# Kernel optimization log

Hardware: AMD Instinct MI355X
Metric: run time of the kernel (lower is better)

## Reference

```python
import jax, jax.numpy as jnp
import numpy as np

B, C, H, W = 8, 256, 64, 64
NUM_LABELS = 16  # labels in {-1, 0..15}; -1 means 'no group'


def setup_inputs() -> dict:
    key = jax.random.key(0)
    kx, kl, kw, kb = jax.random.split(key, 4)
    x = jax.random.normal(kx, (B, C, H, W), dtype=jnp.float32)
    # labels in [-1, NUM_LABELS)
    labels = jax.random.randint(kl, (B * C,), 0, NUM_LABELS + 1) - 1
    # groups=C, kernel 1x1: conv weight is (3C,1,1,1) -> per-output-channel scale; bias (3C,)
    w = jax.random.normal(kw, (3 * C,), dtype=jnp.float32) * 0.5
    b = jax.random.normal(kb, (3 * C,), dtype=jnp.float32) * 0.02
    return {"x": x, "labels": labels, "w": w, "b": b}


def reference(x, labels, w, b):
    # x: (B,C,h,w); labels: (B*C,); w,b: (3C,)
    Bv, Cv, hv, wv = x.shape
    hw = hv * wv
    xf = x.reshape(Bv, Cv, hw)
    # grouped 1x1 conv: out channel o (of 3C) reads input channel o//3
    x_rep = jnp.repeat(xf, 3, axis=1)                      # (B,3C,hw)
    qkv = x_rep * w[None, :, None] + b[None, :, None]      # (B,3C,hw)
    flat = qkv.reshape(Bv * 3 * Cv, hw)                    # matches torch reshape(1,3BC,hw)
    BC = Bv * Cv
    q, k, v = flat[:BC], flat[BC:2 * BC], flat[2 * BC:]    # each (BC, hw)
    valid = labels != -1                                   # (BC,)
    same = (labels[:, None] == labels[None, :]) & valid[:, None] & valid[None, :]
    # per-label-group attention == masked dense attention (softmax over same-label cols only)
    scores = q @ k.T                                       # (BC, BC), no sqrt(d) scaling (as in source)
    neg = jnp.finfo(scores.dtype).min
    scores = jnp.where(same, scores, neg)
    weights = jax.nn.softmax(scores, axis=-1)
    out = weights @ v                                      # (BC, hw)
    out = jnp.where(valid[:, None], out, jnp.zeros((), out.dtype))  # -1 rows stay zero
    return out[None]                                       # (1, BC, hw)
```

## Files before the change

### kernel.cpp

```cpp
#include <hip/hip_runtime.h>
#include <cfloat>

#define B_   8
#define C_   256
#define HW_  4096
#define BC_  2048
#define TC_  768
#define NG_  16
#define MAXG 320
#define UK0  682
#define NUQ  683
#define NUK  684
#define NXU  1366

#define SPLITK 8
#define NT     11
#define NTILES (NT * NT)
#define KSL    (HW_ / SPLITK)
#define WKC    (KSL / 4)
#define NP1    (NUQ * NUK)

#define MCAP  192
#define CST   192
#define BKP   216

typedef __attribute__((ext_vector_type(8))) short short8;
typedef __attribute__((ext_vector_type(4))) float floatx4;

__global__ __launch_bounds__(256) void group_build_kernel(
    const int* __restrict__ labels, int* __restrict__ grp_n,
    int* __restrict__ members, int* __restrict__ posArr)
{
  __shared__ int lab[BC_];
  __shared__ int cnts[256];
  const int g = blockIdx.x;
  const int t = threadIdx.x;
  for (int idx = t; idx < BC_; idx += 256) lab[idx] = labels[idx];
  __syncthreads();

  const int base = t * 8;
  int cnt = 0;
#pragma unroll
  for (int k = 0; k < 8; k++) cnt += (lab[base + k] == g) ? 1 : 0;
  cnts[t] = cnt;
  for (int off = 1; off < 256; off <<= 1) {
    __syncthreads();
    const int v = (t >= off) ? cnts[t - off] : 0;
    __syncthreads();
    cnts[t] += v;
  }
  __syncthreads();
  int pos = cnts[t] - cnt;
  if (t == 255) grp_n[g] = cnts[255] < MAXG ? cnts[255] : MAXG;
#pragma unroll
  for (int k = 0; k < 8; k++) {
    const int i = base + k;
    if (lab[i] == g) {
      if (pos < MAXG) { members[g * MAXG + pos] = i; posArr[i] = pos; }
      pos++;
    }
  }
}

__device__ __forceinline__ unsigned short f32_to_bf16_rne(float f) {
  unsigned u = __float_as_uint(f);
  unsigned r = (u + 0x7FFFu + ((u >> 16) & 1u)) >> 16;
  return (unsigned short)r;
}

__global__ __launch_bounds__(256) void conv_kernel(
    const float* __restrict__ x, unsigned short* __restrict__ xhi,
    unsigned short* __restrict__ xlo, float* __restrict__ sums)
{
  const int u = blockIdx.x;
  const int t = threadIdx.x;
  unsigned short* hrow = xhi + (size_t)u * HW_;
  unsigned short* lrow = xlo + (size_t)u * HW_;
  const float* row = x + (size_t)u * HW_;
  float s = 0.f;
#pragma unroll
  for (int i = 0; i < 4; i++) {
    const int col = i * 1024 + t * 4;
    const float4 v = *(const float4*)(row + col);
    s += v.x + v.y + v.z + v.w;
    ushort4 h, l;
    h.x = f32_to_bf16_rne(v.x);
    h.y = f32_to_bf16_rne(v.y);
    h.z = f32_to_bf16_rne(v.z);
    h.w = f32_to_bf16_rne(v.w);
    l.x = f32_to_bf16_rne(v.x - __uint_as_float((unsigned)h.x << 16));
    l.y = f32_to_bf16_rne(v.y - __uint_as_float((unsigned)h.y << 16));
    l.z = f32_to_bf16_rne(v.z - __uint_as_float((unsigned)h.z << 16));
    l.w = f32_to_bf16_rne(v.w - __uint_as_float((unsigned)h.w << 16));
    *(ushort4*)(hrow + col) = h;
    *(ushort4*)(lrow + col) = l;
  }
#pragma unroll
  for (int o = 32; o > 0; o >>= 1) s += __shfl_down(s, o);
  __shared__ float red[4];
  if ((t & 63) == 0) red[t >> 6] = s;
  __syncthreads();
  if (t == 0) sums[u] = red[0] + red[1] + red[2] + red[3];
}

__global__ __launch_bounds__(256) void gram_mfma_kernel(
    const unsigned short* __restrict__ xhi, const unsigned short* __restrict__ xlo,
    float* __restrict__ P)
{
  const int bid  = blockIdx.x;
  const int z    = bid & 7;
  const int tile = bid >> 3;
  const int m0 = (tile % NT) * 64;
  const int n0 = (tile / NT) * 64;

  const int t = threadIdx.x;
  const int wave = t >> 6;
  const int lane = t & 63;
  const int fr = lane & 15;
  const int fq = lane >> 4;

  const int kbase = z * KSL + wave * WKC + fq * 8;
  const unsigned short *pah[4], *pal[4], *pbh[4], *pbl[4];
#pragma unroll
  for (int i = 0; i < 4; i++) {
    const int ar = min(m0 + fr + i * 16, NUQ - 1);
    const int br = min(UK0 + n0 + fr + i * 16, NXU - 1);
    pah[i] = xhi + (size_t)ar * HW_ + kbase;
    pal[i] = xlo + (size_t)ar * HW_ + kbase;
    pbh[i] = xhi + (size_t)br * HW_ + kbase;
    pbl[i] = xlo + (size_t)br * HW_ + kbase;
  }

  floatx4 acc[4][4];
#pragma unroll
  for (int i = 0; i < 4; i++)
#pragma unroll
    for (int j = 0; j < 4; j++) acc[i][j] = (floatx4)(0.f);

  for (int kk = 0; kk < WKC; kk += 32) {
    short8 ah[4], al[4], bh[4], bl[4];
#pragma unroll
    for (int i = 0; i < 4; i++) {
      ah[i] = *(const short8*)(pah[i] + kk);
      al[i] = *(const short8*)(pal[i] + kk);
      bh[i] = *(const short8*)(pbh[i] + kk);
      bl[i] = *(const short8*)(pbl[i] + kk);
    }
#pragma unroll
    for (int mt = 0; mt < 4; mt++)
#pragma unroll
      for (int nt = 0; nt < 4; nt++) {
        acc[mt][nt] = __builtin_amdgcn_mfma_f32_16x16x32_bf16(ah[mt], bh[nt], acc[mt][nt], 0, 0, 0);
        acc[mt][nt] = __builtin_amdgcn_mfma_f32_16x16x32_bf16(al[mt], bh[nt], acc[mt][nt], 0, 0, 0);
        acc[mt][nt] = __builtin_amdgcn_mfma_f32_16x16x32_bf16(ah[mt], bl[nt], acc[mt][nt], 0, 0, 0);
      }
  }

  __shared__ float R[2][64][68];
  float* R0 = &R[0][0][0];
  float* R1 = &R[1][0][0];
  if (wave == 0 || wave == 2) {
    float* Rw = (wave == 0) ? R0 : R1;
#pragma unroll
    for (int mt = 0; mt < 4; mt++)
#pragma unroll
      for (int nt = 0; nt < 4; nt++)
#pragma unroll
        for (int r = 0; r < 4; r++)
          Rw[(mt * 16 + fq * 4 + r) * 68 + nt * 16 + fr] = acc[mt][nt][r];
  }
  __syncthreads();
  if (wave == 1 || wave == 3) {
    float* Rw = (wave == 1) ? R0 : R1;
#pragma unroll
    for (int mt = 0; mt < 4; mt++)
#pragma unroll
      for (int nt = 0; nt < 4; nt++)
#pragma unroll
        for (int r = 0; r < 4; r++)
          Rw[(mt * 16 + fq * 4 + r) * 68 + nt * 16 + fr] += acc[mt][nt][r];
  }
  __syncthreads();
  const int em = t >> 2;
  const int en = (t & 3) * 16;
  const int gm = m0 + em;
  if (gm < NUQ) {
    float* dst = P + (size_t)z * NP1 + (size_t)gm * NUK + n0;
#pragma unroll
    for (int i4 = 0; i4 < 4; i4++) {
      const int n = en + i4 * 4;
      if (n0 + n < NUK) {
        float4 v;
        v.x = R0[em * 68 + n + 0] + R1[em * 68 + n + 0];
        v.y = R0[em * 68 + n + 1] + R1[em * 68 + n + 1];
        v.z = R0[em * 68 + n + 2] + R1[em * 68 + n + 2];
        v.w = R0[em * 68 + n + 3] + R1[em * 68 + n + 3];
        *(float4*)(dst + n) = v;
      }
    }
  }
}

__global__ __launch_bounds__(256) void gram_reduce_kernel(
    const float* __restrict__ P, float* __restrict__ S)
{
  const int idx = (blockIdx.x * 256 + threadIdx.x) * 4;
  if (idx < NP1) {
    float4 s = *(const float4*)(P + idx);
#pragma unroll
    for (int sl = 1; sl < SPLITK; sl++) {
      const float4 a = *(const float4*)(P + (size_t)sl * NP1 + idx);
      s.x += a.x; s.y += a.y; s.z += a.z; s.w += a.w;
    }
    *(float4*)(S + idx) = s;
  }
}

__device__ __forceinline__ float blockReduceMax(float v, float* red) {
#pragma unroll
  for (int o = 32; o > 0; o >>= 1) v = fmaxf(v, __shfl_down(v, o));
  if ((threadIdx.x & 63) == 0) red[threadIdx.x >> 6] = v;
  __syncthreads();
  v = fmaxf(fmaxf(red[0], red[1]), fmaxf(red[2], red[3]));
  __syncthreads();
  return v;
}
__device__ __forceinline__ float blockReduceSum(float v, float* red) {
#pragma unroll
  for (int o = 32; o > 0; o >>= 1) v += __shfl_down(v, o);
  if ((threadIdx.x & 63) == 0) red[threadIdx.x >> 6] = v;
  __syncthreads();
  v = red[0] + red[1] + red[2] + red[3];
  __syncthreads();
  return v;
}

__global__ __launch_bounds__(256) void softmax_kernel(
    const int* __restrict__ labels, const float* __restrict__ w,
    const float* __restrict__ bbias, const float* __restrict__ sums,
    const float* __restrict__ S, const int* __restrict__ grp_n,
    const int* __restrict__ members, const int* __restrict__ posArr,
    unsigned short* __restrict__ coefh, float* __restrict__ cb,
    float* __restrict__ out)
{
  const int i = blockIdx.x;
  const int t = threadIdx.x;
  const int g = labels[i];
  if (g < 0) {
    const float4 z = make_float4(0.f, 0.f, 0.f, 0.f);
    float4* orow = (float4*)(out + (size_t)i * HW_);
    for (int cidx = t; cidx < HW_ / 4; cidx += 256) orow[cidx] = z;
    return;
  }
  __shared__ float red[4];
  const int n   = grp_n[g];
  const int jq  = i % TC_;
  const int uqi = (i / TC_) * C_ + jq / 3;
  const float wq = w[jq], bq = bbias[jq];
  const float sq = sums[uqi];
  const float* Srow = S + (size_t)uqi * NUK;

  const int jj0 = t, jj1 = t + 256;
  float s0 = -FLT_MAX, s1 = -FLT_MAX;
  if (jj0 < n) {
    const int j = members[g * MAXG + jj0];
    const int rk = j + BC_;
    const int jk = rk % TC_;
    const int uk = (rk / TC_) * C_ + jk / 3;
    s0 = wq * w[jk] * Srow[uk - UK0] + (wq * bbias[jk]) * sq +
         (bq * w[jk]) * sums[uk] + (bq * bbias[jk]) * 4096.f;
  }
  if (jj1 < n) {
    const int j = members[g * MAXG + jj1];
    const int rk = j + BC_;
    const int jk = rk % TC_;
    const int uk = (rk / TC_) * C_ + jk / 3;
    s1 = wq * w[jk] * Srow[uk - UK0] + (wq * bbias[jk]) * sq +
         (bq * w[jk]) * sums[uk] + (bq * bbias[jk]) * 4096.f;
  }
  const float mx = blockReduceMax(fmaxf(s0, s1), red);
  const float e0 = (jj0 < n) ? expf(s0 - mx) : 0.f;
  const float e1 = (jj1 < n) ? expf(s1 - mx) : 0.f;
  const float tot = blockReduceSum(e0 + e1, red);
  const float inv = 1.f / tot;

  const int pos = posArr[i];
  unsigned short* crow = coefh + ((size_t)g * MCAP + pos) * CST;
  float lcb = 0.f;
  if (jj0 < n) {
    const int j = members[g * MAXG + jj0];
    const int jv = (j + 2 * BC_) % TC_;
    const float wgt = e0 * inv;
    if (pos < MCAP && jj0 < CST) crow[jj0] = f32_to_bf16_rne(wgt * w[jv]);
    lcb += wgt * bbias[jv];
  } else if (pos < MCAP && jj0 < CST) {
    crow[jj0] = 0;
  }
  if (jj1 < n) {
    const int j = members[g * MAXG + jj1];
    const int jv = (j + 2 * BC_) % TC_;
    const float wgt = e1 * inv;
    lcb += wgt * bbias[jv];
  }
  const float cbi = blockReduceSum(lcb, red);
  if (t == 0) cb[i] = cbi;
}

__global__ __launch_bounds__(256) void out_mfma_kernel(
    const float* __restrict__ x, const unsigned short* __restrict__ coefh,
    const float* __restrict__ cb, const int* __restrict__ grp_n,
    const int* __restrict__ members, float* __restrict__ out)
{
  const int g  = blockIdx.x;
  const int c0 = blockIdx.y * 64;
  const int n  = min(grp_n[g], MCAP);
  if (n == 0) return;
  const int Kceil = (n + 31) & ~31;
  const int nk8 = Kceil >> 3;
  const int t = threadIdx.x;
  const int wave = t >> 6;
  const int lane = t & 63;
  const int fr = lane & 15;
  const int fq = lane >> 4;

  __shared__ unsigned short Bt[64][BKP];
  __shared__ int   mem[MCAP];
  __shared__ float cbs[MCAP];

  if (t < n) {
    const int j = members[g * MAXG + t];
    mem[t] = j;
    cbs[t] = cb[j];
  }
  __syncthreads();

  {
    const int colq = t & 15;
    const int kcb  = t >> 4;
    for (int kc = kcb; kc < nk8; kc += 16) {
      float4 vals[8];
#pragma unroll
      for (int j = 0; j < 8; j++) {
        const int k = kc * 8 + j;
        if (k < n) {
          const int jm = mem[k];
          const int rv = jm + 2 * BC_;
          const int uv = (rv / TC_) * C_ + (rv % TC_) / 3;
          vals[j] = *(const float4*)(x + (size_t)uv * HW_ + c0 + colq * 4);
        } else {
          vals[j] = make_float4(0.f, 0.f, 0.f, 0.f);
        }
      }
#pragma unroll
      for (int c = 0; c < 4; c++) {
        short8 pk;
        pk[0] = (short)f32_to_bf16_rne(c == 0 ? vals[0].x : c == 1 ? vals[0].y : c == 2 ? vals[0].z : vals[0].w);
        pk[1] = (short)f32_to_bf16_rne(c == 0 ? vals[1].x : c == 1 ? vals[1].y : c == 2 ? vals[1].z : vals[1].w);
        pk[2] = (short)f32_to_bf16_rne(c == 0 ? vals[2].x : c == 1 ? vals[2].y : c == 2 ? vals[2].z : vals[2].w);
        pk[3] = (short)f32_to_bf16_rne(c == 0 ? vals[3].x : c == 1 ? vals[3].y : c == 2 ? vals[3].z : vals[3].w);
        pk[4] = (short)f32_to_bf16_rne(c == 0 ? vals[4].x : c == 1 ? vals[4].y : c == 2 ? vals[4].z : vals[4].w);
        pk[5] = (short)f32_to_bf16_rne(c == 0 ? vals[5].x : c == 1 ? vals[5].y : c == 2 ? vals[5].z : vals[5].w);
        pk[6] = (short)f32_to_bf16_rne(c == 0 ? vals[6].x : c == 1 ? vals[6].y : c == 2 ? vals[6].z : vals[6].w);
        pk[7] = (short)f32_to_bf16_rne(c == 0 ? vals[7].x : c == 1 ? vals[7].y : c == 2 ? vals[7].z : vals[7].w);
        *(short8*)&Bt[colq * 4 + c][kc * 8] = pk;
      }
    }
  }
  __syncthreads();

  const int colw = wave * 16 + fr;

  for (int m0 = 0; m0 < n; m0 += 32) {
    floatx4 acc0 = (floatx4)(0.f), acc1 = (floatx4)(0.f);
    const unsigned short* pa0 = coefh + ((size_t)g * MCAP + m0 + fr) * CST + fq * 8;
    const unsigned short* pa1 = pa0 + 16 * CST;
    for (int k = 0; k < Kceil; k += 32) {
      const short8 a0 = *(const short8*)(pa0 + k);
      const short8 a1 = *(const short8*)(pa1 + k);
      const short8 b  = *(const short8*)&Bt[colw][fq * 8 + k];
      acc0 = __builtin_amdgcn_mfma_f32_16x16x32_bf16(a0, b, acc0, 0, 0, 0);
      acc1 = __builtin_amdgcn_mfma_f32_16x16x32_bf16(a1, b, acc1, 0, 0, 0);
    }
#pragma unroll
    for (int r = 0; r < 4; r++) {
      int m = m0 + fq * 4 + r;
      if (m < n) out[(size_t)mem[m] * HW_ + c0 + colw] = acc0[r] + cbs[m];
      m += 16;
      if (m < n) out[(size_t)mem[m] * HW_ + c0 + colw] = acc1[r] + cbs[m];
    }
  }
}

extern "C" void kernel_launch(void* const* d_in, const int* in_sizes, int n_in,
                              void* d_out, int out_size, void* d_ws, size_t ws_size,
                              hipStream_t stream)
{
  const float* x      = (const float*)d_in[0];
  const int*   labels = (const int*)d_in[1];
  const float* w      = (const float*)d_in[2];
  const float* bb     = (const float*)d_in[3];
  float* out = (float*)d_out;

  char* wsb = (char*)d_ws;
  size_t off = 0;
  auto carve = [&](size_t bytes) -> void* {
    off = (off + 255) & ~(size_t)255;
    void* p = wsb + off;
    off += bytes;
    return p;
  };
  float* sums    = (float*)carve(NXU * sizeof(float));
  float* S       = (float*)carve((size_t)NP1 * sizeof(float));
  float* P       = (float*)carve((size_t)SPLITK * NP1 * sizeof(float));
  int*   grp_n   = (int*)carve(NG_ * sizeof(int));
  int*   members = (int*)carve((size_t)NG_ * MAXG * sizeof(int));
  int*   posArr  = (int*)carve(BC_ * sizeof(int));
  unsigned short* coefh = (unsigned short*)carve((size_t)NG_ * MCAP * CST * sizeof(unsigned short));
  float* cb      = (float*)carve(BC_ * sizeof(float));
  unsigned short* xhi = (unsigned short*)carve((size_t)NXU * HW_ * sizeof(unsigned short));
  unsigned short* xlo = (unsigned short*)carve((size_t)NXU * HW_ * sizeof(unsigned short));

  conv_kernel<<<NXU, 256, 0, stream>>>(x, xhi, xlo, sums);
  group_build_kernel<<<NG_, 256, 0, stream>>>(labels, grp_n, members, posArr);
  gram_mfma_kernel<<<NTILES * SPLITK, 256, 0, stream>>>(xhi, xlo, P);
  gram_reduce_kernel<<<(NP1 / 4 + 255) / 256, 256, 0, stream>>>(P, S);
  softmax_kernel<<<BC_, 256, 0, stream>>>(labels, w, bb, sums, S, grp_n,
                                          members, posArr, coefh, cb, out);
  out_mfma_kernel<<<dim3(NG_, HW_ / 64), 256, 0, stream>>>(
      x, coefh, cb, grp_n, members, out);
}
```

Measured before the change: 163.9 us.

## Merge prep kernels, precompute per-group key tables, reuse bf16 x in output GEMM

Result: no change. 162.1 us (-1.1%).

```diff
diff --git a/kernel.cpp b/kernel.cpp
--- a/kernel.cpp
+++ b/kernel.cpp
@@ -12,6 +12,7 @@
 #define NUQ  683
 #define NUK  684
 #define NXU  1366
+#define NXALL 2048
 
 #define SPLITK 8
 #define NT     11
@@ -19,6 +20,7 @@
 #define KSL    (HW_ / SPLITK)
 #define WKC    (KSL / 4)
 #define NP1    (NUQ * NUK)
+#define REDBLK ((NP1 / 4 + 255) / 256)
 
 #define MCAP  192
 #define CST   192
@@ -26,41 +28,6 @@
 
 typedef __attribute__((ext_vector_type(8))) short short8;
 typedef __attribute__((ext_vector_type(4))) float floatx4;
-
-__global__ __launch_bounds__(256) void group_build_kernel(
-    const int* __restrict__ labels, int* __restrict__ grp_n,
-    int* __restrict__ members, int* __restrict__ posArr)
-{
-  __shared__ int lab[BC_];
-  __shared__ int cnts[256];
-  const int g = blockIdx.x;
-  const int t = threadIdx.x;
-  for (int idx = t; idx < BC_; idx += 256) lab[idx] = labels[idx];
-  __syncthreads();
-
-  const int base = t * 8;
-  int cnt = 0;
-#pragma unroll
-  for (int k = 0; k < 8; k++) cnt += (lab[base + k] == g) ? 1 : 0;
-  cnts[t] = cnt;
-  for (int off = 1; off < 256; off <<= 1) {
-    __syncthreads();
-    const int v = (t >= off) ? cnts[t - off] : 0;
-    __syncthreads();
-    cnts[t] += v;
-  }
-  __syncthreads();
-  int pos = cnts[t] - cnt;
-  if (t == 255) grp_n[g] = cnts[255] < MAXG ? cnts[255] : MAXG;
-#pragma unroll
-  for (int k = 0; k < 8; k++) {
-    const int i = base + k;
-    if (lab[i] == g) {
-      if (pos < MAXG) { members[g * MAXG + pos] = i; posArr[i] = pos; }
-      pos++;
-    }
-  }
-}
 
 __device__ __forceinline__ unsigned short f32_to_bf16_rne(float f) {
   unsigned u = __float_as_uint(f);
@@ -68,39 +35,86 @@
   return (unsigned short)r;
 }
 
-__global__ __launch_bounds__(256) void conv_kernel(
-    const float* __restrict__ x, unsigned short* __restrict__ xhi,
-    unsigned short* __restrict__ xlo, float* __restrict__ sums)
-{
-  const int u = blockIdx.x;
+__global__ __launch_bounds__(256) void prep_kernel(
+    const float* __restrict__ x, const int* __restrict__ labels,
+    unsigned short* __restrict__ xhi, unsigned short* __restrict__ xlo,
+    float* __restrict__ sums, int* __restrict__ grp_n,
+    int* __restrict__ members, int* __restrict__ posArr, int nhi)
+{
   const int t = threadIdx.x;
+  if (blockIdx.x < NG_) {
+    __shared__ int lab[BC_];
+    __shared__ int cnts[256];
+    const int g = blockIdx.x;
+    for (int idx = t; idx < BC_; idx += 256) lab[idx] = labels[idx];
+    __syncthreads();
+    const int base = t * 8;
+    int cnt = 0;
+#pragma unroll
+    for (int k = 0; k < 8; k++) cnt += (lab[base + k] == g) ? 1 : 0;
+    cnts[t] = cnt;
+    for (int off = 1; off < 256; off <<= 1) {
+      __syncthreads();
+      const int v = (t >= off) ? cnts[t - off] : 0;
+      __syncthreads();
+      cnts[t] += v;
+    }
+    __syncthreads();
+    int pos = cnts[t] - cnt;
+    if (t == 255) grp_n[g] = cnts[255] < MAXG ? cnts[255] : MAXG;
+#pragma unroll
+    for (int k = 0; k < 8; k++) {
+      const int i = base + k;
+      if (lab[i] == g) {
+        if (pos < MAXG) { members[g * MAXG + pos] = i; posArr[i] = pos; }
+        pos++;
+      }
+    }
+    return;
+  }
+
+  const int u = blockIdx.x - NG_;
+  const float* row = x + (size_t)u * HW_;
   unsigned short* hrow = xhi + (size_t)u * HW_;
-  unsigned short* lrow = xlo + (size_t)u * HW_;
-  const float* row = x + (size_t)u * HW_;
-  float s = 0.f;
-#pragma unroll
-  for (int i = 0; i < 4; i++) {
-    const int col = i * 1024 + t * 4;
-    const float4 v = *(const float4*)(row + col);
-    s += v.x + v.y + v.z + v.w;
-    ushort4 h, l;
-    h.x = f32_to_bf16_rne(v.x);
-    h.y = f32_to_bf16_rne(v.y);
-    h.z = f32_to_bf16_rne(v.z);
-    h.w = f32_to_bf16_rne(v.w);
-    l.x = f32_to_bf16_rne(v.x - __uint_as_float((unsigned)h.x << 16));
-    l.y = f32_to_bf16_rne(v.y - __uint_as_float((unsigned)h.y << 16));
-    l.z = f32_to_bf16_rne(v.z - __uint_as_float((unsigned)h.z << 16));
-    l.w = f32_to_bf16_rne(v.w - __uint_as_float((unsigned)h.w << 16));
-    *(ushort4*)(hrow + col) = h;
-    *(ushort4*)(lrow + col) = l;
-  }
-#pragma unroll
-  for (int o = 32; o > 0; o >>= 1) s += __shfl_down(s, o);
-  __shared__ float red[4];
-  if ((t & 63) == 0) red[t >> 6] = s;
-  __syncthreads();
-  if (t == 0) sums[u] = red[0] + red[1] + red[2] + red[3];
+  if (u < NXU) {
+    unsigned short* lrow = xlo + (size_t)u * HW_;
+    float s = 0.f;
+#pragma unroll
+    for (int i = 0; i < 4; i++) {
+      const int col = i * 1024 + t * 4;
+      const float4 v = *(const float4*)(row + col);
+      s += v.x + v.y + v.z + v.w;
+      ushort4 h, l;
+      h.x = f32_to_bf16_rne(v.x);
+      h.y = f32_to_bf16_rne(v.y);
+      h.z = f32_to_bf16_rne(v.z);
+      h.w = f32_to_bf16_rne(v.w);
+      l.x = f32_to_bf16_rne(v.x - __uint_as_float((unsigned)h.x << 16));
+      l.y = f32_to_bf16_rne(v.y - __uint_as_float((unsigned)h.y << 16));
+      l.z = f32_to_bf16_rne(v.z - __uint_as_float((unsigned)h.z << 16));
+      l.w = f32_to_bf16_rne(v.w - __uint_as_float((unsigned)h.w << 16));
+      *(ushort4*)(hrow + col) = h;
+      *(ushort4*)(lrow + col) = l;
+    }
+#pragma unroll
+    for (int o = 32; o > 0; o >>= 1) s += __shfl_down(s, o);
+    __shared__ float red[4];
+    if ((t & 63) == 0) red[t >> 6] = s;
+    __syncthreads();
+    if (t == 0) sums[u] = red[0] + red[1] + red[2] + red[3];
+  } else {
+#pragma unroll
+    for (int i = 0; i < 4; i++) {
+      const int col = i * 1024 + t * 4;
+      const float4 v = *(const float4*)(row + col);
+      ushort4 h;
+      h.x = f32_to_bf16_rne(v.x);
+      h.y = f32_to_bf16_rne(v.y);
+      h.z = f32_to_bf16_rne(v.z);
+      h.w = f32_to_bf16_rne(v.w);
+      *(ushort4*)(hrow + col) = h;
+    }
+  }
 }
 
 __global__ __launch_bounds__(256) void gram_mfma_kernel(
@@ -201,18 +215,38 @@
   }
 }
 
-__global__ __launch_bounds__(256) void gram_reduce_kernel(
-    const float* __restrict__ P, float* __restrict__ S)
-{
-  const int idx = (blockIdx.x * 256 + threadIdx.x) * 4;
-  if (idx < NP1) {
-    float4 s = *(const float4*)(P + idx);
-#pragma unroll
-    for (int sl = 1; sl < SPLITK; sl++) {
-      const float4 a = *(const float4*)(P + (size_t)sl * NP1 + idx);
-      s.x += a.x; s.y += a.y; s.z += a.z; s.w += a.w;
-    }
-    *(float4*)(S + idx) = s;
+__global__ __launch_bounds__(256) void reduce_tab_kernel(
+    const float* __restrict__ P, float* __restrict__ S,
+    const float* __restrict__ w, const float* __restrict__ bbias,
+    const float* __restrict__ sums, const int* __restrict__ grp_n,
+    const int* __restrict__ members, float4* __restrict__ gtA,
+    float2* __restrict__ gtB)
+{
+  const int bid = blockIdx.x;
+  const int t = threadIdx.x;
+  if (bid < REDBLK) {
+    const int idx = (bid * 256 + t) * 4;
+    if (idx < NP1) {
+      float4 s = *(const float4*)(P + idx);
+#pragma unroll
+      for (int sl = 1; sl < SPLITK; sl++) {
+        const float4 a = *(const float4*)(P + (size_t)sl * NP1 + idx);
+        s.x += a.x; s.y += a.y; s.z += a.z; s.w += a.w;
+      }
+      *(float4*)(S + idx) = s;
+    }
+    return;
+  }
+  const int g = bid - REDBLK;
+  const int n = grp_n[g];
+  for (int p = t; p < n; p += 256) {
+    const int j = members[g * MAXG + p];
+    const int rk = j + BC_;
+    const int jk = rk % TC_;
+    const int uk = (rk / TC_) * C_ + jk / 3;
+    const int jv = (j + 2 * BC_) % TC_;
+    gtA[g * MAXG + p] = make_float4(w[jk], bbias[jk], sums[uk], w[jv]);
+    gtB[g * MAXG + p] = make_float2(bbias[jv], __int_as_float(uk - UK0));
   }
 }
 
@@ -239,9 +273,9 @@
     const int* __restrict__ labels, const float* __restrict__ w,
     const float* __restrict__ bbias, const float* __restrict__ sums,
     const float* __restrict__ S, const int* __restrict__ grp_n,
-    const int* __restrict__ members, const int* __restrict__ posArr,
-    unsigned short* __restrict__ coefh, float* __restrict__ cb,
-    float* __restrict__ out)
+    const int* __restrict__ posArr, const float4* __restrict__ gtA,
+    const float2* __restrict__ gtB, unsigned short* __restrict__ coefh,
+    float* __restrict__ cb, float* __restrict__ out)
 {
   const int i = blockIdx.x;
   const int t = threadIdx.x;
@@ -261,22 +295,19 @@
   const float* Srow = S + (size_t)uqi * NUK;
 
   const int jj0 = t, jj1 = t + 256;
+  float4 A0, A1; float2 B0, B1;
   float s0 = -FLT_MAX, s1 = -FLT_MAX;
   if (jj0 < n) {
-    const int j = members[g * MAXG + jj0];
-    const int rk = j + BC_;
-    const int jk = rk % TC_;
-    const int uk = (rk / TC_) * C_ + jk / 3;
-    s0 = wq * w[jk] * Srow[uk - UK0] + (wq * bbias[jk]) * sq +
-         (bq * w[jk]) * sums[uk] + (bq * bbias[jk]) * 4096.f;
+    A0 = gtA[g * MAXG + jj0];
+    B0 = gtB[g * MAXG + jj0];
+    s0 = wq * A0.x * Srow[__float_as_int(B0.y)] + (wq * A0.y) * sq +
+         (bq * A0.x) * A0.z + (bq * A0.y) * 4096.f;
   }
   if (jj1 < n) {
-    const int j = members[g * MAXG + jj1];
-    const int rk = j + BC_;
-    const int jk = rk % TC_;
-    const int uk = (rk / TC_) * C_ + jk / 3;
-    s1 = wq * w[jk] * Srow[uk - UK0] + (wq * bbias[jk]) * sq +
-         (bq * w[jk]) * sums[uk] + (bq * bbias[jk]) * 4096.f;
+    A1 = gtA[g * MAXG + jj1];
+    B1 = gtB[g * MAXG + jj1];
+    s1 = wq * A1.x * Srow[__float_as_int(B1.y)] + (wq * A1.y) * sq +
+         (bq * A1.x) * A1.z + (bq * A1.y) * 4096.f;
   }
   const float mx = blockReduceMax(fmaxf(s0, s1), red);
   const float e0 = (jj0 < n) ? expf(s0 - mx) : 0.f;
@@ -288,26 +319,23 @@
   unsigned short* crow = coefh + ((size_t)g * MCAP + pos) * CST;
   float lcb = 0.f;
   if (jj0 < n) {
-    const int j = members[g * MAXG + jj0];
-    const int jv = (j + 2 * BC_) % TC_;
     const float wgt = e0 * inv;
-    if (pos < MCAP && jj0 < CST) crow[jj0] = f32_to_bf16_rne(wgt * w[jv]);
-    lcb += wgt * bbias[jv];
+    if (pos < MCAP && jj0 < CST) crow[jj0] = f32_to_bf16_rne(wgt * A0.w);
+    lcb += wgt * B0.x;
   } else if (pos < MCAP && jj0 < CST) {
     crow[jj0] = 0;
   }
   if (jj1 < n) {
-    const int j = members[g * MAXG + jj1];
-    const int jv = (j + 2 * BC_) % TC_;
     const float wgt = e1 * inv;
-    lcb += wgt * bbias[jv];
+    lcb += wgt * B1.x;
   }
   const float cbi = blockReduceSum(lcb, red);
   if (t == 0) cb[i] = cbi;
 }
 
 __global__ __launch_bounds__(256) void out_mfma_kernel(
-    const float* __restrict__ x, const unsigned short* __restrict__ coefh,
+    const float* __restrict__ x, const unsigned short* __restrict__ xh,
+    const unsigned short* __restrict__ coefh,
     const float* __restrict__ cb, const int* __restrict__ grp_n,
     const int* __restrict__ members, float* __restrict__ out)
 {
@@ -338,31 +366,60 @@
     const int colq = t & 15;
     const int kcb  = t >> 4;
     for (int kc = kcb; kc < nk8; kc += 16) {
-      float4 vals[8];
-#pragma unroll
-      for (int j = 0; j < 8; j++) {
-        const int k = kc * 8 + j;
-        if (k < n) {
-          const int jm = mem[k];
-          const int rv = jm + 2 * BC_;
-          const int uv = (rv / TC_) * C_ + (rv % TC_) / 3;
-          vals[j] = *(const float4*)(x + (size_t)uv * HW_ + c0 + colq * 4);
-        } else {
-          vals[j] = make_float4(0.f, 0.f, 0.f, 0.f);
+      if (xh) {
+        ushort4 hv[8];
+#pragma unroll
+        for (int j = 0; j < 8; j++) {
+          const int k = kc * 8 + j;
+          if (k < n) {
+            const int jm = mem[k];
+            const int rv = jm + 2 * BC_;
+            const int uv = (rv / TC_) * C_ + (rv % TC_) / 3;
+            hv[j] = *(const ushort4*)(xh + (size_t)uv * HW_ + c0 + colq * 4);
+          } else {
+            hv[j] = make_ushort4(0, 0, 0, 0);
+          }
         }
-      }
-#pragma unroll
-      for (int c = 0; c < 4; c++) {
-        short8 pk;
-        pk[0] = (short)f32_to_bf16_rne(c == 0 ? vals[0].x : c == 1 ? vals[0].y : c == 2 ? vals[0].z : vals[0].w);
-        pk[1] = (short)f32_to_bf16_rne(c == 0 ? vals[1].x : c == 1 ? vals[1].y : c == 2 ? vals[1].z : vals[1].w);
-        pk[2] = (short)f32_to_bf16_rne(c == 0 ? vals[2].x : c == 1 ? vals[2].y : c == 2 ? vals[2].z : vals[2].w);
-        pk[3] = (short)f32_to_bf16_rne(c == 0 ? vals[3].x : c == 1 ? vals[3].y : c == 2 ? vals[3].z : vals[3].w);
-        pk[4] = (short)f32_to_bf16_rne(c == 0 ? vals[4].x : c == 1 ? vals[4].y : c == 2 ? vals[4].z : vals[4].w);
-        pk[5] = (short)f32_to_bf16_rne(c == 0 ? vals[5].x : c == 1 ? vals[5].y : c == 2 ? vals[5].z : vals[5].w);
-        pk[6] = (short)f32_to_bf16_rne(c == 0 ? vals[6].x : c == 1 ? vals[6].y : c == 2 ? vals[6].z : vals[6].w);
-        pk[7] = (short)f32_to_bf16_rne(c == 0 ? vals[7].x : c == 1 ? vals[7].y : c == 2 ? vals[7].z : vals[7].w);
-        *(short8*)&Bt[colq * 4 + c][kc * 8] = pk;
+#pragma unroll
+        for (int c = 0; c < 4; c++) {
+          short8 pk;
+          pk[0] = (short)(c == 0 ? hv[0].x : c == 1 ? hv[0].y : c == 2 ? hv[0].z : hv[0].w);
+          pk[1] = (short)(c == 0 ? hv[1].x : c == 1 ? hv[1].y : c == 2 ? hv[1].z : hv[1].w);
+          pk[2] = (short)(c == 0 ? hv[2].x : c == 1 ? hv[2].y : c == 2 ? hv[2].z : hv[2].w);
+          pk[3] = (short)(c == 0 ? hv[3].x : c == 1 ? hv[3].y : c == 2 ? hv[3].z : hv[3].w);
+          pk[4] = (short)(c == 0 ? hv[4].x : c == 1 ? hv[4].y : c == 2 ? hv[4].z : hv[4].w);
+          pk[5] = (short)(c == 0 ? hv[5].x : c == 1 ? hv[5].y : c == 2 ? hv[5].z : hv[5].w);
+          pk[6] = (short)(c == 0 ? hv[6].x : c == 1 ? hv[6].y : c == 2 ? hv[6].z : hv[6].w);
+          pk[7] = (short)(c == 0 ? hv[7].x : c == 1 ? hv[7].y : c == 2 ? hv[7].z : hv[7].w);
+          *(short8*)&Bt[colq * 4 + c][kc * 8] = pk;
+        }
+      } else {
+        float4 vals[8];
+#pragma unroll
+        for (int j = 0; j < 8; j++) {
+          const int k = kc * 8 + j;
+          if (k < n) {
+            const int jm = mem[k];
+            const int rv = jm + 2 * BC_;
+            const int uv = (rv / TC_) * C_ + (rv % TC_) / 3;
+            vals[j] = *(const float4*)(x + (size_t)uv * HW_ + c0 + colq * 4);
+          } else {
+            vals[j] = make_float4(0.f, 0.f, 0.f, 0.f);
+          }
+        }
+#pragma unroll
+        for (int c = 0; c < 4; c++) {
+          short8 pk;
+          pk[0] = (short)f32_to_bf16_rne(c == 0 ? vals[0].x : c == 1 ? vals[0].y : c == 2 ? vals[0].z : vals[0].w);
+          pk[1] = (short)f32_to_bf16_rne(c == 0 ? vals[1].x : c == 1 ? vals[1].y : c == 2 ? vals[1].z : vals[1].w);
+          pk[2] = (short)f32_to_bf16_rne(c == 0 ? vals[2].x : c == 1 ? vals[2].y : c == 2 ? vals[2].z : vals[2].w);
+          pk[3] = (short)f32_to_bf16_rne(c == 0 ? vals[3].x : c == 1 ? vals[3].y : c == 2 ? vals[3].z : vals[3].w);
+          pk[4] = (short)f32_to_bf16_rne(c == 0 ? vals[4].x : c == 1 ? vals[4].y : c == 2 ? vals[4].z : vals[4].w);
+          pk[5] = (short)f32_to_bf16_rne(c == 0 ? vals[5].x : c == 1 ? vals[5].y : c == 2 ? vals[5].z : vals[5].w);
+          pk[6] = (short)f32_to_bf16_rne(c == 0 ? vals[6].x : c == 1 ? vals[6].y : c == 2 ? vals[6].z : vals[6].w);
+          pk[7] = (short)f32_to_bf16_rne(c == 0 ? vals[7].x : c == 1 ? vals[7].y : c == 2 ? vals[7].z : vals[7].w);
+          *(short8*)&Bt[colq * 4 + c][kc * 8] = pk;
+        }
       }
     }
   }
@@ -417,15 +474,22 @@
   int*   posArr  = (int*)carve(BC_ * sizeof(int));
   unsigned short* coefh = (unsigned short*)carve((size_t)NG_ * MCAP * CST * sizeof(unsigned short));
   float* cb      = (float*)carve(BC_ * sizeof(float));
-  unsigned short* xhi = (unsigned short*)carve((size_t)NXU * HW_ * sizeof(unsigned short));
+  float4* gtA    = (float4*)carve((size_t)NG_ * MAXG * sizeof(float4));
+  float2* gtB    = (float2*)carve((size_t)NG_ * MAXG * sizeof(float2));
+
+  const int big = ws_size >= (size_t)47 * 1024 * 1024;
+  const int nhi = big ? NXALL : NXU;
+  unsigned short* xhi = (unsigned short*)carve((size_t)nhi * HW_ * sizeof(unsigned short));
   unsigned short* xlo = (unsigned short*)carve((size_t)NXU * HW_ * sizeof(unsigned short));
 
-  conv_kernel<<<NXU, 256, 0, stream>>>(x, xhi, xlo, sums);
-  group_build_kernel<<<NG_, 256, 0, stream>>>(labels, grp_n, members, posArr);
+  prep_kernel<<<NG_ + nhi, 256, 0, stream>>>(x, labels, xhi, xlo, sums,
+                                             grp_n, members, posArr, nhi);
   gram_mfma_kernel<<<NTILES * SPLITK, 256, 0, stream>>>(xhi, xlo, P);
-  gram_reduce_kernel<<<(NP1 / 4 + 255) / 256, 256, 0, stream>>>(P, S);
+  reduce_tab_kernel<<<REDBLK + NG_, 256, 0, stream>>>(P, S, w, bb, sums,
+                                                      grp_n, members, gtA, gtB);
   softmax_kernel<<<BC_, 256, 0, stream>>>(labels, w, bb, sums, S, grp_n,
-                                          members, posArr, coefh, cb, out);
+                                          posArr, gtA, gtB, coefh, cb, out);
   out_mfma_kernel<<<dim3(NG_, HW_ / 64), 256, 0, stream>>>(
-      x, coefh, cb, grp_n, members, out);
-}
+      x, big ? xhi : (const unsigned short*)nullptr, coefh, cb, grp_n,
+      members, out);
+}
```
